# Kernel tuning notes

Measured on AMD Instinct MI355X. Metric: run time of the kernel, lower is better.

The kernel has to match this reference:

```python
import jax, jax.numpy as jnp
import numpy as np

NUM_USERS = 100000
NUM_ITEMS = 100000
D = 64
C = 9          # cat_num (9 attention layers)
B = 2048       # batch of users
L = 200        # max history length (padded with -1)
H = 16         # attention MLP hidden size


def setup_inputs() -> dict:
    key = jax.random.key(0)
    ks = jax.random.split(key, 12)
    w_range = np.sqrt(3.0 / D).astype(np.float32)

    user_inputs = jax.random.randint(ks[0], (B,), 0, NUM_USERS)
    record = jax.random.randint(ks[1], (B, L), 0, NUM_ITEMS)
    # ragged lengths: pad tail with -1 (original code breaks at -1)
    lengths = jax.random.randint(ks[2], (B, 1), L // 4, L + 1)
    record_inputs = jnp.where(jnp.arange(L)[None, :] < lengths, record, -1)
    item_inputs = jax.random.randint(ks[3], (B,), 0, NUM_ITEMS)
    item_cat = jax.random.randint(ks[4], (NUM_ITEMS,), 0, C)

    user_emb = 0.01 * jax.random.normal(ks[5], (NUM_USERS, D), jnp.float32)
    item_emb = 0.01 * jax.random.normal(ks[6], (NUM_ITEMS, D), jnp.float32)
    W1 = jax.random.uniform(ks[7], (C, H, 2 * D), jnp.float32, -w_range, w_range)
    b1 = jnp.zeros((C, H), jnp.float32)
    W2 = jax.random.uniform(ks[8], (C, 1, H), jnp.float32, -w_range, w_range)
    b2 = jnp.zeros((C, 1), jnp.float32)
    Wt1 = jax.random.uniform(ks[9], (H, 2 * D), jnp.float32, -w_range, w_range)
    bt1 = jnp.zeros((H,), jnp.float32)
    Wt2 = jax.random.uniform(ks[10], (1, H), jnp.float32, -w_range, w_range)
    bt2 = jnp.zeros((1,), jnp.float32)

    return {"user_inputs": user_inputs, "record_inputs": record_inputs,
            "item_inputs": item_inputs, "item_cat": item_cat,
            "user_emb": user_emb, "item_emb": item_emb,
            "W1": W1, "b1": b1, "W2": W2, "b2": b2,
            "Wt1": Wt1, "bt1": bt1, "Wt2": Wt2, "bt2": bt2}


def _forward(user_inputs, record_inputs, item_inputs, item_cat,
             user_emb, item_emb, W1, b1, W2, b2, Wt1, bt1, Wt2, bt2):
    tiny = jnp.asarray(1e-30, jnp.float32)
    valid = record_inputs >= 0                     # [B,L]
    rec = jnp.where(valid, record_inputs, 0)
    e = item_emb[rec]                              # [B,L,D]
    u = user_emb[user_inputs]                      # [B,D]
    x = jnp.concatenate([jnp.broadcast_to(u[:, None, :], e.shape), e], -1)  # [B,L,2D]

    # per-category attention MLP scores (C small -> compute all, gather by cat)
    h = jax.nn.relu(jnp.einsum('chi,bli->bclh', W1, x) + b1[None, :, None, :])  # [B,C,L,H]
    s = jnp.einsum('ch,bclh->bcl', W2[:, 0, :], h) + b2[:, 0][None, :, None]    # [B,C,L]

    cat = item_cat[rec]                                            # [B,L]
    member = (cat[:, None, :] == jnp.arange(C)[None, :, None]) & valid[:, None, :]  # [B,C,L]

    # masked softmax within each (user, category) group
    smax = jnp.max(jnp.where(member, s, -jnp.inf), axis=-1, keepdims=True)
    smax = jnp.where(jnp.isfinite(smax), smax, 0.0)
    z = jnp.where(member, jnp.exp(s - smax), 0.0)
    w = z / jnp.maximum(jnp.sum(z, -1, keepdims=True), tiny)       # [B,C,L]
    gvec = jnp.einsum('bcl,bld->bcd', w, e)                        # [B,C,D]
    group_has = jnp.any(member, axis=-1)                           # [B,C]

    # top-level attention over non-empty groups
    x2 = jnp.concatenate([jnp.broadcast_to(u[:, None, :], gvec.shape), gvec], -1)  # [B,C,2D]
    h2 = jax.nn.relu(jnp.einsum('hi,bci->bch', Wt1, x2) + bt1)      # [B,C,H]
    s2 = jnp.einsum('h,bch->bc', Wt2[0], h2) + bt2[0]               # [B,C]
    s2max = jnp.max(jnp.where(group_has, s2, -jnp.inf), -1, keepdims=True)
    s2max = jnp.where(jnp.isfinite(s2max), s2max, 0.0)
    z2 = jnp.where(group_has, jnp.exp(s2 - s2max), 0.0)
    w2 = z2 / jnp.maximum(jnp.sum(z2, -1, keepdims=True), tiny)
    hybrid = jnp.einsum('bc,bcd->bd', w2, gvec)                     # [B,D]

    ti = item_emb[item_inputs]                                      # [B,D]
    return jnp.sum(hybrid * ti, -1).reshape(-1, 1, 1)               # [B,1,1]


def reference(user_inputs, record_inputs, item_inputs, item_cat,
              user_emb, item_emb, W1, b1, W2, b2, Wt1, bt1, Wt2, bt2):
    return _forward(user_inputs, record_inputs, item_inputs, item_cat,
                    user_emb, item_emb, W1, b1, W2, b2, Wt1, bt1, Wt2, bt2)
```

## Files before the change

kernel.cpp:

```cpp
#include <hip/hip_runtime.h>
#include <math.h>

#define NB 2048
#define LL 200
#define PADL 256
#define DD 64
#define CC 9
#define HH 16
#define NW 4


__global__ __launch_bounds__(256) void din_ka(
    const int* __restrict__ user_inputs,
    const int* __restrict__ record_inputs,
    const int* __restrict__ item_cat,
    const float* __restrict__ user_emb,
    const float* __restrict__ W1,
    const float* __restrict__ b1,
    int* __restrict__ srow_g,
    int* __restrict__ cstart_g,
    float* __restrict__ pre_g)
{
  const int b = blockIdx.x;
  const int t = threadIdx.x;
  const int wave = t >> 6, lane = t & 63;

  __shared__ float u_s[DD];
  __shared__ int   wcnt[NW][CC];
  __shared__ int   cstart[CC + 1];
  __shared__ int   ccnt[CC];

  int r = -1, c0 = -1;
  if (t < LL) {
    r = record_inputs[b * LL + t];
    if (r >= 0) c0 = item_cat[r];
  }
  if (t < DD) u_s[t] = user_emb[(size_t)user_inputs[b] * DD + t];

  srow_g[b * PADL + t] = 0;

  int myrank = 0;
  #pragma unroll
  for (int c = 0; c < CC; ++c) {
    unsigned long long m = __ballot(c0 == c);
    if (lane == 0) wcnt[wave][c] = __popcll(m);
    if (c0 == c) myrank = __popcll(m & ((1ULL << lane) - 1ULL));
  }
  __syncthreads();

  if (t == 0) {
    int acc = 0;
    #pragma unroll
    for (int c = 0; c < CC; ++c) {
      cstart[c] = acc;
      int cn = wcnt[0][c] + wcnt[1][c] + wcnt[2][c] + wcnt[3][c];
      ccnt[c] = cn;
      acc = (acc + cn + 3) & ~3;
    }
    cstart[CC] = acc;
  }
  if (t < CC * HH) {
    int c = t / HH, j = t % HH;
    const float* wp = &W1[(size_t)(c * HH + j) * (2 * DD)];
    float acc = b1[c * HH + j];
    #pragma unroll 8
    for (int d = 0; d < DD; ++d) acc += wp[d] * u_s[d];
    pre_g[(size_t)(b * CC + c) * HH + j] = acc;
  }
  __syncthreads();

  if (c0 >= 0) {
    int off = cstart[c0];
    for (int w = 0; w < wave; ++w) off += wcnt[w][c0];
    srow_g[b * PADL + off + myrank] = r;
  }
  if (t < CC + 1) cstart_g[b * 20 + t] = cstart[t];
  else if (t < 2 * CC + 1) cstart_g[b * 20 + 10 + (t - CC - 1)] = ccnt[t - CC - 1];
}

__global__ __launch_bounds__(256) void din_kb(
    const float* __restrict__ item_emb,
    const float* __restrict__ W1,
    const float* __restrict__ W2,
    const float* __restrict__ b2,
    const int* __restrict__ srow_g,
    const int* __restrict__ cstart_g,
    const float* __restrict__ pre_g,
    float* __restrict__ z_g)
{
  const int t = threadIdx.x;

  __shared__ float4 w_lds[HH * 16 * CC];
  __shared__ float  w2_s[CC * HH];
  __shared__ float  b2_s[CC];

  #pragma unroll
  for (int k = t; k < HH * 16 * CC; k += 256) {
    int c = k >> 8;
    int ji = k & 255;
    int j = ji >> 4, i = ji & 15;
    w_lds[ji * CC + c] = ((const float4*)W1)[(size_t)(c * HH + j) * 32 + 16 + i];
  }
  if (t < CC * HH) w2_s[t] = W2[t];
  if (t < CC) b2_s[t] = b2[t];
  __syncthreads();

  const int gid = blockIdx.x * 256 + t;
  const int b   = gid >> 7;
  const int pt  = gid & 127;
  const int grp = pt >> 1;
  const int jh  = pt & 1;
  const int q4  = grp * 4;
  const int* cs = &cstart_g[b * 20];
  if (q4 >= cs[CC]) return;

  int c = 0;
  #pragma unroll
  for (int q = 0; q < CC - 1; ++q) c += (q4 >= cs[q + 1]) ? 1 : 0;

  const int base = b * PADL + q4;
  const int r0 = srow_g[base + 0], r1 = srow_g[base + 1];
  const int r2 = srow_g[base + 2], r3 = srow_g[base + 3];
  const float4* e0 = (const float4*)&item_emb[(size_t)r0 * DD];
  const float4* e1 = (const float4*)&item_emb[(size_t)r1 * DD];
  const float4* e2 = (const float4*)&item_emb[(size_t)r2 * DD];
  const float4* e3 = (const float4*)&item_emb[(size_t)r3 * DD];

  float acc0[8], acc1[8], acc2[8], acc3[8];
  {
    const float* pp = &pre_g[(size_t)(b * CC + c) * HH + jh * 8];
    #pragma unroll
    for (int jj = 0; jj < 8; ++jj) {
      float pv = pp[jj];
      acc0[jj] = pv; acc1[jj] = pv; acc2[jj] = pv; acc3[jj] = pv;
    }
  }

  #pragma unroll
  for (int i = 0; i < 16; ++i) {
    float4 a0 = e0[i], a1 = e1[i], a2 = e2[i], a3 = e3[i];
    #pragma unroll
    for (int jj = 0; jj < 8; ++jj) {
      float4 wv = w_lds[((jh * 8 + jj) * 16 + i) * CC + c];
      acc0[jj] += wv.x * a0.x + wv.y * a0.y + wv.z * a0.z + wv.w * a0.w;
      acc1[jj] += wv.x * a1.x + wv.y * a1.y + wv.z * a1.z + wv.w * a1.w;
      acc2[jj] += wv.x * a2.x + wv.y * a2.y + wv.z * a2.z + wv.w * a2.w;
      acc3[jj] += wv.x * a3.x + wv.y * a3.y + wv.z * a3.z + wv.w * a3.w;
    }
  }

  float s0 = 0.f, s1 = 0.f, s2 = 0.f, s3 = 0.f;
  #pragma unroll
  for (int jj = 0; jj < 8; ++jj) {
    float w2v = w2_s[c * HH + jh * 8 + jj];
    s0 += w2v * fmaxf(acc0[jj], 0.f);
    s1 += w2v * fmaxf(acc1[jj], 0.f);
    s2 += w2v * fmaxf(acc2[jj], 0.f);
    s3 += w2v * fmaxf(acc3[jj], 0.f);
  }
  s0 += __shfl_xor(s0, 1, 64);
  s1 += __shfl_xor(s1, 1, 64);
  s2 += __shfl_xor(s2, 1, 64);
  s3 += __shfl_xor(s3, 1, 64);

  if (jh == 0) {
    const float b2c = b2_s[c];
    *(float4*)&z_g[base] = make_float4(expf(s0 + b2c), expf(s1 + b2c),
                                       expf(s2 + b2c), expf(s3 + b2c));
  }
}

__global__ __launch_bounds__(256) void din_kcd(
    const int* __restrict__ user_inputs,
    const int* __restrict__ item_inputs,
    const float* __restrict__ user_emb,
    const float* __restrict__ item_emb,
    const float* __restrict__ Wt1,
    const float* __restrict__ bt1,
    const float* __restrict__ Wt2,
    const float* __restrict__ bt2,
    const int* __restrict__ srow_g,
    const float* __restrict__ z_g,
    const int* __restrict__ cstart_g,
    float* __restrict__ out)
{
  const int b = blockIdx.x;
  const int t = threadIdx.x;
  const int wave = t >> 6, lane = t & 63;
  const int g = lane >> 4;
  const int h = lane & 15;

  __shared__ float u_s[DD];
  __shared__ float gvec_s[CC][DD];
  __shared__ float h2_s[CC][HH];
  __shared__ float w2t_s[CC];
  __shared__ int   cnt_s[CC];

  if (t < DD) u_s[t] = user_emb[(size_t)user_inputs[b] * DD + t];

  for (int c = wave; c < CC; c += NW) {
    const int i0 = cstart_g[b * 20 + c];
    const int n  = cstart_g[b * 20 + 10 + c];
    if (lane == 0) cnt_s[c] = n;
    const int sb = b * PADL + i0;

    float4 acc = make_float4(0.f, 0.f, 0.f, 0.f);
    float  zs  = 0.f;

    for (int cb = 0; cb < n; cb += 64) {
      const int nn = min(64, n - cb);
      const bool ok = (cb + lane) < n;
      int   rv = ok ? srow_g[sb + cb + lane] : 0;
      float zv = ok ? z_g[sb + cb + lane]    : 0.f;
      zs += zv;

      const int kmax = (nn + 3) >> 2;
      #pragma unroll 4
      for (int k = 0; k < kmax; ++k) {
        const int j = 4 * k + g;
        const int   rr = __shfl(rv, j, 64);
        const float zz = __shfl(zv, j, 64);
        const float4 ev = *(const float4*)&item_emb[(size_t)rr * DD + 4 * h];
        acc.x += zz * ev.x; acc.y += zz * ev.y;
        acc.z += zz * ev.z; acc.w += zz * ev.w;
      }
    }

    acc.x += __shfl_xor(acc.x, 16, 64); acc.y += __shfl_xor(acc.y, 16, 64);
    acc.z += __shfl_xor(acc.z, 16, 64); acc.w += __shfl_xor(acc.w, 16, 64);
    acc.x += __shfl_xor(acc.x, 32, 64); acc.y += __shfl_xor(acc.y, 32, 64);
    acc.z += __shfl_xor(acc.z, 32, 64); acc.w += __shfl_xor(acc.w, 32, 64);
    #pragma unroll
    for (int off = 32; off > 0; off >>= 1) zs += __shfl_xor(zs, off, 64);

    if (g == 0) {
      const float inv = 1.f / fmaxf(zs, 1e-30f);
      gvec_s[c][4 * h + 0] = acc.x * inv;
      gvec_s[c][4 * h + 1] = acc.y * inv;
      gvec_s[c][4 * h + 2] = acc.z * inv;
      gvec_s[c][4 * h + 3] = acc.w * inv;
    }
  }
  __syncthreads();

  if (t < CC * HH) {
    int cc = t / HH, j = t % HH;
    const float* wp = &Wt1[(size_t)j * (2 * DD)];
    float a = bt1[j];
    #pragma unroll 8
    for (int d = 0; d < DD; ++d) a += wp[d] * u_s[d];
    #pragma unroll 8
    for (int d = 0; d < DD; ++d) a += wp[DD + d] * gvec_s[cc][d];
    h2_s[cc][j] = fmaxf(a, 0.f);
  }
  __syncthreads();

  if (t == 0) {
    float s2[CC];
    float m = -INFINITY;
    #pragma unroll
    for (int cc = 0; cc < CC; ++cc) {
      float a = bt2[0];
      #pragma unroll
      for (int j = 0; j < HH; ++j) a += Wt2[j] * h2_s[cc][j];
      s2[cc] = a;
      if (cnt_s[cc] > 0) m = fmaxf(m, a);
    }
    if (m == -INFINITY) m = 0.f;
    float sum = 0.f;
    float z2[CC];
    #pragma unroll
    for (int cc = 0; cc < CC; ++cc) {
      z2[cc] = (cnt_s[cc] > 0) ? expf(s2[cc] - m) : 0.f;
      sum += z2[cc];
    }
    float inv = 1.f / fmaxf(sum, 1e-30f);
    #pragma unroll
    for (int cc = 0; cc < CC; ++cc) w2t_s[cc] = z2[cc] * inv;
  }
  __syncthreads();

  if (t < DD) {
    float hy = 0.f;
    #pragma unroll
    for (int cc = 0; cc < CC; ++cc) hy += w2t_s[cc] * gvec_s[cc][t];
    float ti = item_emb[(size_t)item_inputs[b] * DD + t];
    float prod = hy * ti;
    #pragma unroll
    for (int off = 32; off > 0; off >>= 1)
      prod += __shfl_down(prod, off, 64);
    if (t == 0) out[b] = prod;
  }
}

extern "C" void kernel_launch(void* const* d_in, const int* in_sizes, int n_in,
                              void* d_out, int out_size, void* d_ws, size_t ws_size,
                              hipStream_t stream) {
  const int*   user_inputs   = (const int*)d_in[0];
  const int*   record_inputs = (const int*)d_in[1];
  const int*   item_inputs   = (const int*)d_in[2];
  const int*   item_cat      = (const int*)d_in[3];
  const float* user_emb      = (const float*)d_in[4];
  const float* item_emb      = (const float*)d_in[5];
  const float* W1            = (const float*)d_in[6];
  const float* b1            = (const float*)d_in[7];
  const float* W2            = (const float*)d_in[8];
  const float* b2            = (const float*)d_in[9];
  const float* Wt1           = (const float*)d_in[10];
  const float* bt1           = (const float*)d_in[11];
  const float* Wt2           = (const float*)d_in[12];
  const float* bt2           = (const float*)d_in[13];
  float* out = (float*)d_out;

  char* ws = (char*)d_ws;
  int*   srow_g   = (int*)(ws);
  float* z_g      = (float*)(ws + 2097152);
  int*   cstart_g = (int*)(ws + 4194304);
  float* pre_g    = (float*)(ws + 4358144);

  din_ka<<<NB, 256, 0, stream>>>(user_inputs, record_inputs, item_cat,
                                 user_emb, W1, b1, srow_g, cstart_g, pre_g);
  din_kb<<<NB / 2, 256, 0, stream>>>(item_emb, W1, W2, b2,
                                     srow_g, cstart_g, pre_g, z_g);
  din_kcd<<<NB, 256, 0, stream>>>(user_inputs, item_inputs, user_emb, item_emb,
                                  Wt1, bt1, Wt2, bt2,
                                  srow_g, z_g, cstart_g, out);
}
```

Baseline: 78.84 us.

## Fuse category bucketing and per-item attention scoring into one kernel

Merges the bucketing kernel and the per-item MLP scoring kernel into a single per-batch-row kernel. The sorted record indices and the user-dependent pre-activation now stay in shared memory instead of round-tripping through global workspace, and one launch is removed. Each block now handles one user with four threads per item group splitting the hidden units, which changes work distribution and requires every block to stage the full W1 item half into LDS. This extra per-block weight load and larger LDS footprint may reduce occupancy.

```diff
diff --git a/kernel.cpp b/kernel.cpp
--- a/kernel.cpp
+++ b/kernel.cpp
@@ -10,25 +10,43 @@
 #define NW 4
 
 
-__global__ __launch_bounds__(256) void din_ka(
+__global__ __launch_bounds__(256) void din_k1(
     const int* __restrict__ user_inputs,
     const int* __restrict__ record_inputs,
     const int* __restrict__ item_cat,
     const float* __restrict__ user_emb,
+    const float* __restrict__ item_emb,
     const float* __restrict__ W1,
     const float* __restrict__ b1,
+    const float* __restrict__ W2,
+    const float* __restrict__ b2,
     int* __restrict__ srow_g,
-    int* __restrict__ cstart_g,
-    float* __restrict__ pre_g)
+    float* __restrict__ z_g,
+    int* __restrict__ cstart_g)
 {
   const int b = blockIdx.x;
   const int t = threadIdx.x;
   const int wave = t >> 6, lane = t & 63;
 
-  __shared__ float u_s[DD];
-  __shared__ int   wcnt[NW][CC];
-  __shared__ int   cstart[CC + 1];
-  __shared__ int   ccnt[CC];
+  __shared__ float4 w_lds[HH * 16 * CC];
+  __shared__ float  w2_s[CC * HH];
+  __shared__ float  b2_s[CC];
+  __shared__ float  u_s[DD];
+  __shared__ float  pre_s[CC][HH];
+  __shared__ int    wcnt[NW][CC];
+  __shared__ int    cstart[CC + 1];
+  __shared__ int    ccnt[CC];
+  __shared__ int    srow_sh[PADL];
+
+  #pragma unroll
+  for (int k = t; k < HH * 16 * CC; k += 256) {
+    int c = k >> 8;
+    int ji = k & 255;
+    int j = ji >> 4, i = ji & 15;
+    w_lds[ji * CC + c] = ((const float4*)W1)[(size_t)(c * HH + j) * 32 + 16 + i];
+  }
+  if (t < CC * HH) w2_s[t] = W2[t];
+  if (t < CC) b2_s[t] = b2[t];
 
   int r = -1, c0 = -1;
   if (t < LL) {
@@ -36,7 +54,7 @@
     if (r >= 0) c0 = item_cat[r];
   }
   if (t < DD) u_s[t] = user_emb[(size_t)user_inputs[b] * DD + t];
-
+  srow_sh[t] = 0;
   srow_g[b * PADL + t] = 0;
 
   int myrank = 0;
@@ -65,108 +83,76 @@
     float acc = b1[c * HH + j];
     #pragma unroll 8
     for (int d = 0; d < DD; ++d) acc += wp[d] * u_s[d];
-    pre_g[(size_t)(b * CC + c) * HH + j] = acc;
+    pre_s[c][j] = acc;
   }
   __syncthreads();
 
   if (c0 >= 0) {
     int off = cstart[c0];
     for (int w = 0; w < wave; ++w) off += wcnt[w][c0];
-    srow_g[b * PADL + off + myrank] = r;
+    int pos = off + myrank;
+    srow_sh[pos] = r;
+    srow_g[b * PADL + pos] = r;
   }
   if (t < CC + 1) cstart_g[b * 20 + t] = cstart[t];
   else if (t < 2 * CC + 1) cstart_g[b * 20 + 10 + (t - CC - 1)] = ccnt[t - CC - 1];
-}
-
-__global__ __launch_bounds__(256) void din_kb(
-    const float* __restrict__ item_emb,
-    const float* __restrict__ W1,
-    const float* __restrict__ W2,
-    const float* __restrict__ b2,
-    const int* __restrict__ srow_g,
-    const int* __restrict__ cstart_g,
-    const float* __restrict__ pre_g,
-    float* __restrict__ z_g)
-{
-  const int t = threadIdx.x;
-
-  __shared__ float4 w_lds[HH * 16 * CC];
-  __shared__ float  w2_s[CC * HH];
-  __shared__ float  b2_s[CC];
-
-  #pragma unroll
-  for (int k = t; k < HH * 16 * CC; k += 256) {
-    int c = k >> 8;
-    int ji = k & 255;
-    int j = ji >> 4, i = ji & 15;
-    w_lds[ji * CC + c] = ((const float4*)W1)[(size_t)(c * HH + j) * 32 + 16 + i];
-  }
-  if (t < CC * HH) w2_s[t] = W2[t];
-  if (t < CC) b2_s[t] = b2[t];
-  __syncthreads();
-
-  const int gid = blockIdx.x * 256 + t;
-  const int b   = gid >> 7;
-  const int pt  = gid & 127;
-  const int grp = pt >> 1;
-  const int jh  = pt & 1;
-  const int q4  = grp * 4;
-  const int* cs = &cstart_g[b * 20];
-  if (q4 >= cs[CC]) return;
-
-  int c = 0;
-  #pragma unroll
-  for (int q = 0; q < CC - 1; ++q) c += (q4 >= cs[q + 1]) ? 1 : 0;
-
-  const int base = b * PADL + q4;
-  const int r0 = srow_g[base + 0], r1 = srow_g[base + 1];
-  const int r2 = srow_g[base + 2], r3 = srow_g[base + 3];
-  const float4* e0 = (const float4*)&item_emb[(size_t)r0 * DD];
-  const float4* e1 = (const float4*)&item_emb[(size_t)r1 * DD];
-  const float4* e2 = (const float4*)&item_emb[(size_t)r2 * DD];
-  const float4* e3 = (const float4*)&item_emb[(size_t)r3 * DD];
-
-  float acc0[8], acc1[8], acc2[8], acc3[8];
-  {
-    const float* pp = &pre_g[(size_t)(b * CC + c) * HH + jh * 8];
-    #pragma unroll
-    for (int jj = 0; jj < 8; ++jj) {
-      float pv = pp[jj];
+  __syncthreads();
+
+  const int ntot = cstart[CC];
+  const int grp  = t >> 2;
+  const int jq   = t & 3;
+  const int q4   = grp * 4;
+  if (q4 < ntot) {
+    int c = 0;
+    #pragma unroll
+    for (int q = 0; q < CC - 1; ++q) c += (q4 >= cstart[q + 1]) ? 1 : 0;
+
+    const int r0 = srow_sh[q4 + 0], r1 = srow_sh[q4 + 1];
+    const int r2 = srow_sh[q4 + 2], r3 = srow_sh[q4 + 3];
+    const float4* e0 = (const float4*)&item_emb[(size_t)r0 * DD];
+    const float4* e1 = (const float4*)&item_emb[(size_t)r1 * DD];
+    const float4* e2 = (const float4*)&item_emb[(size_t)r2 * DD];
+    const float4* e3 = (const float4*)&item_emb[(size_t)r3 * DD];
+
+    float acc0[4], acc1[4], acc2[4], acc3[4];
+    #pragma unroll
+    for (int jj = 0; jj < 4; ++jj) {
+      float pv = pre_s[c][jq * 4 + jj];
       acc0[jj] = pv; acc1[jj] = pv; acc2[jj] = pv; acc3[jj] = pv;
     }
-  }
-
-  #pragma unroll
-  for (int i = 0; i < 16; ++i) {
-    float4 a0 = e0[i], a1 = e1[i], a2 = e2[i], a3 = e3[i];
-    #pragma unroll
-    for (int jj = 0; jj < 8; ++jj) {
-      float4 wv = w_lds[((jh * 8 + jj) * 16 + i) * CC + c];
-      acc0[jj] += wv.x * a0.x + wv.y * a0.y + wv.z * a0.z + wv.w * a0.w;
-      acc1[jj] += wv.x * a1.x + wv.y * a1.y + wv.z * a1.z + wv.w * a1.w;
-      acc2[jj] += wv.x * a2.x + wv.y * a2.y + wv.z * a2.z + wv.w * a2.w;
-      acc3[jj] += wv.x * a3.x + wv.y * a3.y + wv.z * a3.z + wv.w * a3.w;
-    }
-  }
-
-  float s0 = 0.f, s1 = 0.f, s2 = 0.f, s3 = 0.f;
-  #pragma unroll
-  for (int jj = 0; jj < 8; ++jj) {
-    float w2v = w2_s[c * HH + jh * 8 + jj];
-    s0 += w2v * fmaxf(acc0[jj], 0.f);
-    s1 += w2v * fmaxf(acc1[jj], 0.f);
-    s2 += w2v * fmaxf(acc2[jj], 0.f);
-    s3 += w2v * fmaxf(acc3[jj], 0.f);
-  }
-  s0 += __shfl_xor(s0, 1, 64);
-  s1 += __shfl_xor(s1, 1, 64);
-  s2 += __shfl_xor(s2, 1, 64);
-  s3 += __shfl_xor(s3, 1, 64);
-
-  if (jh == 0) {
-    const float b2c = b2_s[c];
-    *(float4*)&z_g[base] = make_float4(expf(s0 + b2c), expf(s1 + b2c),
-                                       expf(s2 + b2c), expf(s3 + b2c));
+
+    #pragma unroll
+    for (int i = 0; i < 16; ++i) {
+      float4 a0 = e0[i], a1 = e1[i], a2 = e2[i], a3 = e3[i];
+      #pragma unroll
+      for (int jj = 0; jj < 4; ++jj) {
+        float4 wv = w_lds[((jq * 4 + jj) * 16 + i) * CC + c];
+        acc0[jj] += wv.x * a0.x + wv.y * a0.y + wv.z * a0.z + wv.w * a0.w;
+        acc1[jj] += wv.x * a1.x + wv.y * a1.y + wv.z * a1.z + wv.w * a1.w;
+        acc2[jj] += wv.x * a2.x + wv.y * a2.y + wv.z * a2.z + wv.w * a2.w;
+        acc3[jj] += wv.x * a3.x + wv.y * a3.y + wv.z * a3.z + wv.w * a3.w;
+      }
+    }
+
+    float s0 = 0.f, s1 = 0.f, s2 = 0.f, s3 = 0.f;
+    #pragma unroll
+    for (int jj = 0; jj < 4; ++jj) {
+      float w2v = w2_s[c * HH + jq * 4 + jj];
+      s0 += w2v * fmaxf(acc0[jj], 0.f);
+      s1 += w2v * fmaxf(acc1[jj], 0.f);
+      s2 += w2v * fmaxf(acc2[jj], 0.f);
+      s3 += w2v * fmaxf(acc3[jj], 0.f);
+    }
+    s0 += __shfl_xor(s0, 1, 64); s0 += __shfl_xor(s0, 2, 64);
+    s1 += __shfl_xor(s1, 1, 64); s1 += __shfl_xor(s1, 2, 64);
+    s2 += __shfl_xor(s2, 1, 64); s2 += __shfl_xor(s2, 2, 64);
+    s3 += __shfl_xor(s3, 1, 64); s3 += __shfl_xor(s3, 2, 64);
+
+    if (jq == 0) {
+      const float b2c = b2_s[c];
+      *(float4*)&z_g[b * PADL + q4] = make_float4(expf(s0 + b2c), expf(s1 + b2c),
+                                                  expf(s2 + b2c), expf(s3 + b2c));
+    }
   }
 }
 
@@ -316,12 +302,10 @@
   int*   srow_g   = (int*)(ws);
   float* z_g      = (float*)(ws + 2097152);
   int*   cstart_g = (int*)(ws + 4194304);
-  float* pre_g    = (float*)(ws + 4358144);
-
-  din_ka<<<NB, 256, 0, stream>>>(user_inputs, record_inputs, item_cat,
-                                 user_emb, W1, b1, srow_g, cstart_g, pre_g);
-  din_kb<<<NB / 2, 256, 0, stream>>>(item_emb, W1, W2, b2,
-                                     srow_g, cstart_g, pre_g, z_g);
+
+  din_k1<<<NB, 256, 0, stream>>>(user_inputs, record_inputs, item_cat,
+                                 user_emb, item_emb, W1, b1, W2, b2,
+                                 srow_g, z_g, cstart_g);
   din_kcd<<<NB, 256, 0, stream>>>(user_inputs, item_inputs, user_emb, item_emb,
                                   Wt1, bt1, Wt2, bt2,
                                   srow_g, z_g, cstart_g, out);
```

Measured after the change: 70.38 us. 10.7% less time.
